# Performance work log

Measured on AMD Instinct MI355X. Metric: run time of the kernel, lower is better.

The kernel has to match this reference:

```python
import jax, jax.numpy as jnp
import numpy as np

N = 100000      # nodes
E = 1600000     # edges
G = 256         # graphs in the batch
D_IN = 128
H = 128
C = 10
EPS = 1e-5      # BatchNorm eps


def setup_inputs() -> dict:
    key = jax.random.key(0)
    ks = jax.random.split(key, 32)
    inp = {
        'x': jax.random.normal(ks[0], (N, D_IN), jnp.float32),
        'edge_index': jax.random.randint(ks[1], (2, E), 0, N, dtype=jnp.int64),
        'batch': jnp.sort(jax.random.randint(ks[2], (N,), 0, G, dtype=jnp.int64)),
        'w1': jax.random.normal(ks[3], (D_IN, H), jnp.float32) * 0.05,
        'b1': jax.random.normal(ks[4], (H,), jnp.float32) * 0.05,
        'w2': jax.random.normal(ks[5], (H, H), jnp.float32) * 0.05,
        'b2': jax.random.normal(ks[6], (H,), jnp.float32) * 0.05,
        'w3': jax.random.normal(ks[7], (H, H), jnp.float32) * 0.05,
        'b3': jax.random.normal(ks[8], (H,), jnp.float32) * 0.05,
        'g1': jax.random.uniform(ks[9], (H,), jnp.float32, 0.5, 1.5),
        'be1': jax.random.normal(ks[10], (H,), jnp.float32) * 0.05,
        'm1': jax.random.normal(ks[11], (H,), jnp.float32) * 0.05,
        'v1': jax.random.uniform(ks[12], (H,), jnp.float32, 0.5, 1.5),
        'g2': jax.random.uniform(ks[13], (H,), jnp.float32, 0.5, 1.5),
        'be2': jax.random.normal(ks[14], (H,), jnp.float32) * 0.05,
        'm2': jax.random.normal(ks[15], (H,), jnp.float32) * 0.05,
        'v2': jax.random.uniform(ks[16], (H,), jnp.float32, 0.5, 1.5),
        'g3': jax.random.uniform(ks[17], (H,), jnp.float32, 0.5, 1.5),
        'be3': jax.random.normal(ks[18], (H,), jnp.float32) * 0.05,
        'm3': jax.random.normal(ks[19], (H,), jnp.float32) * 0.05,
        'v3': jax.random.uniform(ks[20], (H,), jnp.float32, 0.5, 1.5),
        'fcw1': jax.random.normal(ks[21], (H, H // 2), jnp.float32) * 0.05,
        'fcb1': jax.random.normal(ks[22], (H // 2,), jnp.float32) * 0.05,
        'fcw2': jax.random.normal(ks[23], (H // 2, C), jnp.float32) * 0.05,
        'fcb2': jax.random.normal(ks[24], (C,), jnp.float32) * 0.05,
    }
    return inp


def _gcn_norm(edge_index, n_nodes):
    # add self loops (PyG GCNConv default) and compute D^-1/2 (A+I) D^-1/2 norms
    loop = jnp.arange(n_nodes, dtype=edge_index.dtype)
    src = jnp.concatenate([edge_index[0], loop])
    dst = jnp.concatenate([edge_index[1], loop])
    deg = jax.ops.segment_sum(jnp.ones_like(dst, dtype=jnp.float32), dst, num_segments=n_nodes)
    dinv = jnp.where(deg > 0, jax.lax.rsqrt(deg), 0.0)
    norm = dinv[src] * dinv[dst]  # [E+N]
    return src, dst, norm


def _gcn_conv(x, W, b, src, dst, norm, n_nodes):
    h = x @ W                                   # [N, H]
    msg = norm[:, None] * h[src]                # gather + scale, [E+N, H]
    return jax.ops.segment_sum(msg, dst, num_segments=n_nodes) + b


def _bn_eval(x, gamma, beta, mean, var):
    return (x - mean) * jax.lax.rsqrt(var + EPS) * gamma + beta


def reference(x, edge_index, batch, w1, b1, w2, b2, w3, b3,
              g1, be1, m1, v1, g2, be2, m2, v2, g3, be3, m3, v3,
              fcw1, fcb1, fcw2, fcb2):
    n = x.shape[0]
    x = jnp.nan_to_num(x, nan=0.0, posinf=1e6, neginf=-1e6)
    src, dst, norm = _gcn_norm(edge_index, n)

    h = jax.nn.relu(_bn_eval(_gcn_conv(x, w1, b1, src, dst, norm, n), g1, be1, m1, v1))
    h = jax.nn.relu(_bn_eval(_gcn_conv(h, w2, b2, src, dst, norm, n), g2, be2, m2, v2))
    h = jax.nn.relu(_bn_eval(_gcn_conv(h, w3, b3, src, dst, norm, n), g3, be3, m3, v3))

    # global_mean_pool over graphs
    sums = jax.ops.segment_sum(h, batch, num_segments=G)            # [G, H]
    cnts = jax.ops.segment_sum(jnp.ones((n,), h.dtype), batch, num_segments=G)
    pooled = sums / jnp.maximum(cnts, 1.0)[:, None]

    out = jax.nn.relu(pooled @ fcw1 + fcb1) @ fcw2 + fcb2           # [G, C]
    return out
```

## Files before the change

### kernel.cpp

```cpp
#include <hip/hip_runtime.h>
#include <math.h>

#define NN 100000
#define EE 1600000
#define GG 256
#define HH 128
#define BSH 8
#define NBK 391
#define PASSA_WG 391
#define CAPB 5632

typedef __attribute__((ext_vector_type(8))) short short8;
typedef __attribute__((ext_vector_type(4))) float f32x4;

union U4S8 { uint4 u; short8 s; };

static __device__ __forceinline__ unsigned bf16rne(float f) {
    const unsigned u = __float_as_uint(f);
    return (u + 0x7fffu + ((u >> 16) & 1u)) >> 16;
}
static __device__ __forceinline__ unsigned packbf(float a, float b) {
    return bf16rne(a) | (bf16rne(b) << 16);
}
static __device__ __forceinline__ float bflo(unsigned u) { return __uint_as_float(u << 16); }
static __device__ __forceinline__ float bfhi(unsigned u) { return __uint_as_float(u & 0xffff0000u); }

__global__ void detect_k(const int* __restrict__ ei, const int* __restrict__ batch,
                         int* __restrict__ flags) {
    if (threadIdx.x == 0 && blockIdx.x == 0) {
        int e64 = 1;
        for (int j = 0; j < 8; ++j) {
            if (ei[2 * EE - 1 - 2 * j] != 0) { e64 = 0; break; }
        }
        flags[0] = e64;
        flags[1] = (batch[NN - 1] == 0) ? 1 : 0;
    }
}

__global__ __launch_bounds__(512) void cursinit_k(int* __restrict__ cursor) {
    const int b = blockIdx.x * 512 + threadIdx.x;
    if (b < NBK) cursor[b] = b * CAPB;
}

__global__ void bnprep_k(const float* __restrict__ b1, const float* __restrict__ g1,
                         const float* __restrict__ be1, const float* __restrict__ m1,
                         const float* __restrict__ v1,
                         const float* __restrict__ b2, const float* __restrict__ g2,
                         const float* __restrict__ be2, const float* __restrict__ m2,
                         const float* __restrict__ v2,
                         const float* __restrict__ b3, const float* __restrict__ g3,
                         const float* __restrict__ be3, const float* __restrict__ m3,
                         const float* __restrict__ v3,
                         float* __restrict__ sc, float* __restrict__ sh) {
    const int c = threadIdx.x;
    float s;
    s = g1[c] / sqrtf(v1[c] + 1e-5f);
    sc[c] = s;           sh[c] = (b1[c] - m1[c]) * s + be1[c];
    s = g2[c] / sqrtf(v2[c] + 1e-5f);
    sc[128 + c] = s;     sh[128 + c] = (b2[c] - m2[c]) * s + be2[c];
    s = g3[c] / sqrtf(v3[c] + 1e-5f);
    sc[256 + c] = s;     sh[256 + c] = (b3[c] - m3[c]) * s + be3[c];
}

__global__ __launch_bounds__(256) void wprep_k(const float* __restrict__ w1,
                                               const float* __restrict__ w2,
                                               const float* __restrict__ w3,
                                               unsigned* __restrict__ bt) {
    const int id = blockIdx.x * 256 + threadIdx.x;
    if (id >= 3 * 8192) return;
    const int w = id >> 13;
    const int rem = id & 8191;
    const int n = rem >> 6;
    const int kk = rem & 63;
    const float* W = (w == 0) ? w1 : (w == 1) ? w2 : w3;
    bt[id] = packbf(W[(2 * kk) * HH + n], W[(2 * kk + 1) * HH + n]);
}

__global__ __launch_bounds__(256) void passA_k(const int* __restrict__ ei,
                                               const int* __restrict__ flags,
                                               int* __restrict__ cursor,
                                               unsigned* __restrict__ pairs) {
    __shared__ int h[NBK];
    __shared__ int rbase[NBK];
    const int tid = threadIdx.x;
    for (int i = tid; i < NBK; i += 256) h[i] = 0;
    __syncthreads();
    const bool e64 = flags[0] != 0;
    const int base = blockIdx.x * 4096;
    int scache[16], dcache[16];
#pragma unroll
    for (int j = 0; j < 16; ++j) {
        const int e = base + j * 256 + tid;
        int s = -1, d = 0;
        if (e < EE) {
            s = e64 ? ei[2 * e] : ei[e];
            d = e64 ? ei[2 * (EE + e)] : ei[EE + e];
            atomicAdd(&h[d >> BSH], 1);
        }
        scache[j] = s; dcache[j] = d;
    }
    __syncthreads();
    for (int i = tid; i < NBK; i += 256) {
        const int c = h[i];
        rbase[i] = c ? atomicAdd(&cursor[i], c) : 0;
    }
    __syncthreads();
    for (int i = tid; i < NBK; i += 256) h[i] = 0;
    __syncthreads();
#pragma unroll
    for (int j = 0; j < 16; ++j) {
        const int s = scache[j];
        if (s >= 0) {
            const int d = dcache[j];
            const int b = d >> BSH;
            const int r = atomicAdd(&h[b], 1);
            pairs[rbase[b] + r] = ((unsigned)(d & 255) << 17) | (unsigned)s;
        }
    }
}

__global__ __launch_bounds__(256) void passB_k(const unsigned* __restrict__ pairs,
                                               const int* __restrict__ cursor,
                                               int* __restrict__ offs,
                                               int* __restrict__ degcnt,
                                               float* __restrict__ dinv,
                                               int* __restrict__ csr) {
    __shared__ unsigned pk[CAPB];
    __shared__ int cnt[256];
    __shared__ int loff[256];
    __shared__ int sc[256];
    const int tid = threadIdx.x;
    const int b = blockIdx.x;
    const int p0 = b * CAPB;
    const int np = cursor[b] - p0;
    const int nb0 = b << BSH;
    const int nnode = (NN - nb0 < 256) ? (NN - nb0) : 256;

    cnt[tid] = 0;
    __syncthreads();
    for (int i = tid; i < np; i += 256) {
        const unsigned p = pairs[p0 + i];
        pk[i] = p;
        atomicAdd(&cnt[p >> 17], 1);
    }
    __syncthreads();
    const int creal = cnt[tid];
    const int cpad = (tid < nnode) ? ((creal + 4) & ~3) : 0;
    sc[tid] = cpad;
    __syncthreads();
    for (int off = 1; off < 256; off <<= 1) {
        int t = (tid >= off) ? sc[tid - off] : 0;
        __syncthreads();
        sc[tid] += t;
        __syncthreads();
    }
    const int ex = sc[tid] - cpad;
    loff[tid] = ex;
    if (tid < nnode) {
        const int node = nb0 + tid;
        offs[node] = p0 + ex;
        degcnt[node] = creal;
        dinv[node] = 1.0f / sqrtf((float)(creal + 1));
    }
    __syncthreads();
    cnt[tid] = 0;
    __syncthreads();
    for (int i = tid; i < np; i += 256) {
        const unsigned p = pk[i];
        const int dl = (int)(p >> 17);
        const int r = atomicAdd(&cnt[dl], 1);
        csr[p0 + loff[dl] + r] = (int)(p & 0x1FFFFu);
    }
    if (tid < nnode) {
        const int basep = p0 + loff[tid];
        csr[basep + creal] = nb0 + tid;
        for (int j = creal + 1; j < cpad; ++j) csr[basep + j] = NN;
    }
}

static __device__ __forceinline__ float sani(float v) {
    if (isnan(v)) return 0.0f;
    if (isinf(v)) return v > 0.0f ? 1e6f : -1e6f;
    return v;
}

template <bool AF32>
__global__ __launch_bounds__(256) void gemm_mfma_k(const float* __restrict__ Af,
                                                   const unsigned* __restrict__ Abf,
                                                   const unsigned* __restrict__ btg,
                                                   const float* __restrict__ dinv,
                                                   unsigned* __restrict__ C, int M) {
    __shared__ unsigned lds_u[8704];
    const int tid = threadIdx.x;
    const int wave = tid >> 6;
    const int lane = tid & 63;
    const int nl = lane & 15;
    const int q = lane >> 4;

    {
        const uint4* __restrict__ bg4 = (const uint4*)btg;
        for (int i = tid; i < 2048; i += 256) {
            const int n = i >> 4, w4 = i & 15;
            *(uint4*)&lds_u[n * 68 + w4 * 4] = bg4[n * 16 + w4];
        }
    }
    __syncthreads();

    const int row0 = blockIdx.x * 64 + wave * 16;
    const int rowa = min(row0 + nl, M - 1);

    short8 a[4];
    if (AF32) {
#pragma unroll
        for (int ks = 0; ks < 4; ++ks) {
            const float4 p = *(const float4*)(Af + (size_t)rowa * HH + ks * 32 + q * 8);
            const float4 r = *(const float4*)(Af + (size_t)rowa * HH + ks * 32 + q * 8 + 4);
            U4S8 cv;
            cv.u = make_uint4(packbf(sani(p.x), sani(p.y)), packbf(sani(p.z), sani(p.w)),
                              packbf(sani(r.x), sani(r.y)), packbf(sani(r.z), sani(r.w)));
            a[ks] = cv.s;
        }
    } else {
#pragma unroll
        for (int ks = 0; ks < 4; ++ks) {
            U4S8 cv;
            cv.u = *(const uint4*)(Abf + (size_t)rowa * 64 + ks * 16 + q * 4);
            a[ks] = cv.s;
        }
    }

    f32x4 acc[8];
#pragma unroll
    for (int t = 0; t < 8; ++t) acc[t] = (f32x4)0.0f;

    const unsigned short* __restrict__ bts = (const unsigned short*)lds_u;
#pragma unroll
    for (int ks = 0; ks < 4; ++ks) {
#pragma unroll
        for (int t = 0; t < 8; ++t) {
            const int n = t * 16 + nl;
            const short8 b = *(const short8*)(bts + n * 136 + ks * 32 + q * 8);
            acc[t] = __builtin_amdgcn_mfma_f32_16x16x32_bf16(a[ks], b, acc[t], 0, 0, 0);
        }
    }

    __syncthreads();

    float* __restrict__ cs = (float*)lds_u + wave * 16 * 132;
#pragma unroll
    for (int t = 0; t < 8; ++t) {
#pragma unroll
        for (int r = 0; r < 4; ++r) {
            cs[(q * 4 + r) * 132 + t * 16 + nl] = acc[t][r];
        }
    }
    __syncthreads();

    const int rr = lane & 15;
    const int seg = lane >> 4;
    const int rowg = row0 + rr;
    if (rowg < M) {
        const float dsc = dinv[rowg];
        const float4* crow = (const float4*)(cs + rr * 132) + seg * 8;
#pragma unroll
        for (int j = 0; j < 4; ++j) {
            const float4 fa = crow[2 * j];
            const float4 fb = crow[2 * j + 1];
            const uint4 o = make_uint4(packbf(dsc * fa.x, dsc * fa.y),
                                       packbf(dsc * fa.z, dsc * fa.w),
                                       packbf(dsc * fb.x, dsc * fb.y),
                                       packbf(dsc * fb.z, dsc * fb.w));
            *(uint4*)(C + (size_t)rowg * 64 + seg * 16 + j * 4) = o;
        }
    } else if (rowg == M) {
        const uint4 z = make_uint4(0, 0, 0, 0);
#pragma unroll
        for (int j = 0; j < 4; ++j)
            *(uint4*)(C + (size_t)M * 64 + seg * 16 + j * 4) = z;
    }
}

__global__ __launch_bounds__(256) void aggregate_k(
    const unsigned* __restrict__ hpre, const int* __restrict__ csr,
    const int* __restrict__ offs, const int* __restrict__ cnt,
    const float* __restrict__ dinv,
    const float* __restrict__ bnsc, const float* __restrict__ bnsh,
    unsigned* __restrict__ xout) {
    const int v = __builtin_amdgcn_readfirstlane(blockIdx.x * 4 + (threadIdx.x >> 6));
    const int lane = threadIdx.x & 63;
    const int cg = lane & 15;
    const int sub = lane >> 4;
    const int c8 = cg * 8;

    const float dv = dinv[v];
    const int start = offs[v];
    const int npad = (cnt[v] + 4) & ~3;
    const char* __restrict__ hb = (const char*)hpre;
    const unsigned cgo = (unsigned)(cg << 4);

    float acc[8];
#pragma unroll
    for (int j = 0; j < 8; ++j) acc[j] = 0.0f;

    int i = 0;
    for (; i + 8 <= npad; i += 8) {
        const int sA = csr[start + i + sub];
        const int sB = csr[start + i + 4 + sub];
        const uint4 rA = *(const uint4*)(hb + (((unsigned)sA << 8) | cgo));
        const uint4 rB = *(const uint4*)(hb + (((unsigned)sB << 8) | cgo));
        acc[0] += bflo(rA.x) + bflo(rB.x);
        acc[1] += bfhi(rA.x) + bfhi(rB.x);
        acc[2] += bflo(rA.y) + bflo(rB.y);
        acc[3] += bfhi(rA.y) + bfhi(rB.y);
        acc[4] += bflo(rA.z) + bflo(rB.z);
        acc[5] += bfhi(rA.z) + bfhi(rB.z);
        acc[6] += bflo(rA.w) + bflo(rB.w);
        acc[7] += bfhi(rA.w) + bfhi(rB.w);
    }
    if (i < npad) {
        const int s = csr[start + i + sub];
        const uint4 r = *(const uint4*)(hb + (((unsigned)s << 8) | cgo));
        acc[0] += bflo(r.x); acc[1] += bfhi(r.x);
        acc[2] += bflo(r.y); acc[3] += bfhi(r.y);
        acc[4] += bflo(r.z); acc[5] += bfhi(r.z);
        acc[6] += bflo(r.w); acc[7] += bfhi(r.w);
    }

#pragma unroll
    for (int j = 0; j < 8; ++j) {
        acc[j] += __shfl_xor(acc[j], 16);
        acc[j] += __shfl_xor(acc[j], 32);
    }

    if (sub == 0) {
        const float4 sca = *(const float4*)(bnsc + c8);
        const float4 scb = *(const float4*)(bnsc + c8 + 4);
        const float4 sha = *(const float4*)(bnsh + c8);
        const float4 shb = *(const float4*)(bnsh + c8 + 4);
        const float y0 = fmaxf(dv * acc[0] * sca.x + sha.x, 0.0f);
        const float y1 = fmaxf(dv * acc[1] * sca.y + sha.y, 0.0f);
        const float y2 = fmaxf(dv * acc[2] * sca.z + sha.z, 0.0f);
        const float y3 = fmaxf(dv * acc[3] * sca.w + sha.w, 0.0f);
        const float y4 = fmaxf(dv * acc[4] * scb.x + shb.x, 0.0f);
        const float y5 = fmaxf(dv * acc[5] * scb.y + shb.y, 0.0f);
        const float y6 = fmaxf(dv * acc[6] * scb.z + shb.z, 0.0f);
        const float y7 = fmaxf(dv * acc[7] * scb.w + shb.w, 0.0f);
        *(uint4*)(xout + (size_t)v * 64 + cg * 4) =
            make_uint4(packbf(y0, y1), packbf(y2, y3), packbf(y4, y5), packbf(y6, y7));
    }
}

__global__ __launch_bounds__(256) void pool_sum_k(
    const unsigned* __restrict__ x, const int* __restrict__ batch,
    const int* __restrict__ flags, float* __restrict__ psum,
    int* __restrict__ gcnt) {
    const int wave = threadIdx.x >> 6;
    const int lane = threadIdx.x & 63;
    const int row0 = blockIdx.x * 64 + wave * 16;
    if (row0 >= NN) return;
    const bool b64 = flags[1] != 0;

    float sx = 0.0f, sy = 0.0f;
    int cur = -1, runlen = 0;
#pragma unroll
    for (int r = 0; r < 16; ++r) {
        const int row = row0 + r;
        if (row >= NN) break;
        const int g = b64 ? batch[2 * row] : batch[row];
        if (g != cur) {
            if (cur >= 0) {
                atomicAdd(&psum[cur * HH + lane * 2 + 0], sx);
                atomicAdd(&psum[cur * HH + lane * 2 + 1], sy);
                if (lane == 0) atomicAdd(&gcnt[cur], runlen);
            }
            cur = g; sx = 0.0f; sy = 0.0f; runlen = 0;
        }
        const unsigned u = x[(size_t)row * 64 + lane];
        sx += bflo(u);
        sy += bfhi(u);
        ++runlen;
    }
    if (cur >= 0) {
        atomicAdd(&psum[cur * HH + lane * 2 + 0], sx);
        atomicAdd(&psum[cur * HH + lane * 2 + 1], sy);
        if (lane == 0) atomicAdd(&gcnt[cur], runlen);
    }
}

__global__ __launch_bounds__(128) void head_k(
    const float* __restrict__ psum, const int* __restrict__ gcnt,
    const float* __restrict__ fw1, const float* __restrict__ fb1,
    const float* __restrict__ fw2, const float* __restrict__ fb2,
    float* __restrict__ out) {
    __shared__ float pooled[128];
    __shared__ float hid[64];
    const int g = blockIdx.x;
    const int tid = threadIdx.x;

    const int cntn = gcnt[g];
    pooled[tid] = psum[g * HH + tid] / (float)(cntn > 0 ? cntn : 1);
    __syncthreads();

    if (tid < 64) {
        float a = fb1[tid];
#pragma unroll 4
        for (int k = 0; k < 128; ++k) a += pooled[k] * fw1[k * 64 + tid];
        hid[tid] = fmaxf(a, 0.0f);
    }
    __syncthreads();
    if (tid < 10) {
        float a = fb2[tid];
#pragma unroll
        for (int k = 0; k < 64; ++k) a += hid[k] * fw2[k * 10 + tid];
        out[g * 10 + tid] = a;
    }
}

extern "C" void kernel_launch(void* const* d_in, const int* in_sizes, int n_in,
                              void* d_out, int out_size, void* d_ws, size_t ws_size,
                              hipStream_t stream) {
    const float* x_in  = (const float*)d_in[0];
    const int*   ei    = (const int*)d_in[1];
    const int*   batch = (const int*)d_in[2];
    const float* w1 = (const float*)d_in[3];
    const float* b1 = (const float*)d_in[4];
    const float* w2 = (const float*)d_in[5];
    const float* b2 = (const float*)d_in[6];
    const float* w3 = (const float*)d_in[7];
    const float* b3 = (const float*)d_in[8];
    const float* g1 = (const float*)d_in[9];
    const float* be1 = (const float*)d_in[10];
    const float* m1 = (const float*)d_in[11];
    const float* v1 = (const float*)d_in[12];
    const float* g2 = (const float*)d_in[13];
    const float* be2 = (const float*)d_in[14];
    const float* m2 = (const float*)d_in[15];
    const float* v2 = (const float*)d_in[16];
    const float* g3 = (const float*)d_in[17];
    const float* be3 = (const float*)d_in[18];
    const float* m3 = (const float*)d_in[19];
    const float* v3 = (const float*)d_in[20];
    const float* fw1 = (const float*)d_in[21];
    const float* fb1 = (const float*)d_in[22];
    const float* fw2 = (const float*)d_in[23];
    const float* fb2 = (const float*)d_in[24];
    float* out = (float*)d_out;

    size_t off = 0;
    char* base = (char*)d_ws;
    auto alloc = [&](size_t bytes) -> void* {
        void* p = base + off;
        off += (bytes + 255) & ~(size_t)255;
        return p;
    };
    int*      degcnt = (int*)alloc((size_t)NN * 4);
    float*    dinv   = (float*)alloc((size_t)NN * 4);
    int*      offs   = (int*)alloc((size_t)NN * 4);
    int*      cursor = (int*)alloc((size_t)NBK * 4);
    int*      flags  = (int*)alloc(256);
    float*    bnsc   = (float*)alloc(3 * 128 * 4);
    float*    bnsh   = (float*)alloc(3 * 128 * 4);
    unsigned* btg    = (unsigned*)alloc(3 * 8192 * 4);
    float*    psum   = (float*)alloc((size_t)GG * HH * 4);
    int*      gcnt   = (int*)alloc((size_t)GG * 4);
    int*      csr    = (int*)alloc((size_t)NBK * CAPB * 4);
    unsigned* pairs  = (unsigned*)alloc((size_t)NBK * CAPB * 4);
    unsigned* bufx   = (unsigned*)alloc((size_t)NN * 64 * 4);
    unsigned* hpre   = (unsigned*)alloc((size_t)(NN + 1) * 64 * 4);
    if (off > ws_size) return;

    detect_k<<<1, 64, 0, stream>>>(ei, batch, flags);
    cursinit_k<<<1, 512, 0, stream>>>(cursor);
    bnprep_k<<<1, 128, 0, stream>>>(b1, g1, be1, m1, v1,
                                    b2, g2, be2, m2, v2,
                                    b3, g3, be3, m3, v3, bnsc, bnsh);
    wprep_k<<<96, 256, 0, stream>>>(w1, w2, w3, btg);
    hipMemsetAsync(psum, 0, (size_t)GG * HH * 4, stream);
    hipMemsetAsync(gcnt, 0, (size_t)GG * 4, stream);
    passA_k<<<PASSA_WG, 256, 0, stream>>>(ei, flags, cursor, pairs);
    passB_k<<<NBK, 256, 0, stream>>>(pairs, cursor, offs, degcnt, dinv, csr);

    const int ggrid = (NN + 63) / 64;
    const int agrid = NN / 4;

    gemm_mfma_k<true><<<ggrid, 256, 0, stream>>>(x_in, nullptr, btg, dinv, hpre, NN);
    aggregate_k<<<agrid, 256, 0, stream>>>(hpre, csr, offs, degcnt, dinv,
                                           bnsc, bnsh, bufx);
    gemm_mfma_k<false><<<ggrid, 256, 0, stream>>>(nullptr, bufx, btg + 8192, dinv, hpre, NN);
    aggregate_k<<<agrid, 256, 0, stream>>>(hpre, csr, offs, degcnt, dinv,
                                           bnsc + 128, bnsh + 128, bufx);
    gemm_mfma_k<false><<<ggrid, 256, 0, stream>>>(nullptr, bufx, btg + 16384, dinv, hpre, NN);
    aggregate_k<<<agrid, 256, 0, stream>>>(hpre, csr, offs, degcnt, dinv,
                                           bnsc + 256, bnsh + 256, bufx);

    pool_sum_k<<<ggrid, 256, 0, stream>>>(bufx, batch, flags, psum, gcnt);
    head_k<<<GG, 128, 0, stream>>>(psum, gcnt, fw1, fb1, fw2, fb2, out);
}
```

Baseline: 456.5 us.

## Drop LDS staging in MFMA GEMM and unroll aggregation gather to 16 neighbors

The GEMM kernel no longer stages the weight matrix and output tile through shared memory. It reads B fragments straight from global memory and swaps MFMA operands so each lane holds a row-contiguous output that it writes directly as packed bf16. This removes the LDS copies and barriers, at the cost of redundant global/L2 reads of the weights per wave. Separately, CSR rows are padded to multiples of 8 instead of 4 (with a larger per-bucket capacity), so the aggregation loop can issue four independent gathers per iteration for more memory-level parallelism, at the cost of extra padding entries.

New measurement: 506.7 us. 11.0% more time.

```diff
diff --git a/kernel.cpp b/kernel.cpp
--- a/kernel.cpp
+++ b/kernel.cpp
@@ -8,7 +8,7 @@
 #define BSH 8
 #define NBK 391
 #define PASSA_WG 391
-#define CAPB 5632
+#define CAPB 6144
 
 typedef __attribute__((ext_vector_type(8))) short short8;
 typedef __attribute__((ext_vector_type(4))) float f32x4;
@@ -145,7 +145,7 @@
     }
     __syncthreads();
     const int creal = cnt[tid];
-    const int cpad = (tid < nnode) ? ((creal + 4) & ~3) : 0;
+    const int cpad = (tid < nnode) ? ((creal + 8) & ~7) : 0;
     sc[tid] = cpad;
     __syncthreads();
     for (int off = 1; off < 256; off <<= 1) {
@@ -190,24 +190,14 @@
                                                    const unsigned* __restrict__ btg,
                                                    const float* __restrict__ dinv,
                                                    unsigned* __restrict__ C, int M) {
-    __shared__ unsigned lds_u[8704];
     const int tid = threadIdx.x;
     const int wave = tid >> 6;
     const int lane = tid & 63;
     const int nl = lane & 15;
     const int q = lane >> 4;
-
-    {
-        const uint4* __restrict__ bg4 = (const uint4*)btg;
-        for (int i = tid; i < 2048; i += 256) {
-            const int n = i >> 4, w4 = i & 15;
-            *(uint4*)&lds_u[n * 68 + w4 * 4] = bg4[n * 16 + w4];
-        }
-    }
-    __syncthreads();
-
     const int row0 = blockIdx.x * 64 + wave * 16;
-    const int rowa = min(row0 + nl, M - 1);
+    const int rowg = row0 + nl;
+    const int rowa = min(rowg, M - 1);
 
     short8 a[4];
     if (AF32) {
@@ -233,50 +223,33 @@
 #pragma unroll
     for (int t = 0; t < 8; ++t) acc[t] = (f32x4)0.0f;
 
-    const unsigned short* __restrict__ bts = (const unsigned short*)lds_u;
-#pragma unroll
-    for (int ks = 0; ks < 4; ++ks) {
-#pragma unroll
-        for (int t = 0; t < 8; ++t) {
-            const int n = t * 16 + nl;
-            const short8 b = *(const short8*)(bts + n * 136 + ks * 32 + q * 8);
-            acc[t] = __builtin_amdgcn_mfma_f32_16x16x32_bf16(a[ks], b, acc[t], 0, 0, 0);
-        }
-    }
-
-    __syncthreads();
-
-    float* __restrict__ cs = (float*)lds_u + wave * 16 * 132;
+    const uint4* __restrict__ bt4 = (const uint4*)btg;
 #pragma unroll
     for (int t = 0; t < 8; ++t) {
-#pragma unroll
-        for (int r = 0; r < 4; ++r) {
-            cs[(q * 4 + r) * 132 + t * 16 + nl] = acc[t][r];
-        }
-    }
-    __syncthreads();
-
-    const int rr = lane & 15;
-    const int seg = lane >> 4;
-    const int rowg = row0 + rr;
+        const int n = t * 16 + nl;
+#pragma unroll
+        for (int ks = 0; ks < 4; ++ks) {
+            U4S8 cv;
+            cv.u = bt4[n * 16 + ks * 4 + q];
+            acc[t] = __builtin_amdgcn_mfma_f32_16x16x32_bf16(cv.s, a[ks], acc[t], 0, 0, 0);
+        }
+    }
+
     if (rowg < M) {
         const float dsc = dinv[rowg];
-        const float4* crow = (const float4*)(cs + rr * 132) + seg * 8;
-#pragma unroll
-        for (int j = 0; j < 4; ++j) {
-            const float4 fa = crow[2 * j];
-            const float4 fb = crow[2 * j + 1];
-            const uint4 o = make_uint4(packbf(dsc * fa.x, dsc * fa.y),
-                                       packbf(dsc * fa.z, dsc * fa.w),
-                                       packbf(dsc * fb.x, dsc * fb.y),
-                                       packbf(dsc * fb.z, dsc * fb.w));
-            *(uint4*)(C + (size_t)rowg * 64 + seg * 16 + j * 4) = o;
+        unsigned* crow = C + (size_t)rowg * 64;
+#pragma unroll
+        for (int t = 0; t < 8; ++t) {
+            uint2 o;
+            o.x = packbf(dsc * acc[t][0], dsc * acc[t][1]);
+            o.y = packbf(dsc * acc[t][2], dsc * acc[t][3]);
+            *(uint2*)(crow + t * 8 + q * 2) = o;
         }
     } else if (rowg == M) {
-        const uint4 z = make_uint4(0, 0, 0, 0);
-#pragma unroll
-        for (int j = 0; j < 4; ++j)
-            *(uint4*)(C + (size_t)M * 64 + seg * 16 + j * 4) = z;
+        unsigned* crow = C + (size_t)M * 64;
+#pragma unroll
+        for (int t = 0; t < 8; ++t)
+            *(uint2*)(crow + t * 8 + q * 2) = make_uint2(0u, 0u);
     }
 }
 
@@ -294,7 +267,7 @@
 
     const float dv = dinv[v];
     const int start = offs[v];
-    const int npad = (cnt[v] + 4) & ~3;
+    const int npad = (cnt[v] + 8) & ~7;
     const char* __restrict__ hb = (const char*)hpre;
     const unsigned cgo = (unsigned)(cg << 4);
 
@@ -303,7 +276,25 @@
     for (int j = 0; j < 8; ++j) acc[j] = 0.0f;
 
     int i = 0;
-    for (; i + 8 <= npad; i += 8) {
+    for (; i + 16 <= npad; i += 16) {
+        const int sA = csr[start + i + sub];
+        const int sB = csr[start + i + 4 + sub];
+        const int sC = csr[start + i + 8 + sub];
+        const int sD = csr[start + i + 12 + sub];
+        const uint4 rA = *(const uint4*)(hb + (((unsigned)sA << 8) | cgo));
+        const uint4 rB = *(const uint4*)(hb + (((unsigned)sB << 8) | cgo));
+        const uint4 rC = *(const uint4*)(hb + (((unsigned)sC << 8) | cgo));
+        const uint4 rD = *(const uint4*)(hb + (((unsigned)sD << 8) | cgo));
+        acc[0] += (bflo(rA.x) + bflo(rB.x)) + (bflo(rC.x) + bflo(rD.x));
+        acc[1] += (bfhi(rA.x) + bfhi(rB.x)) + (bfhi(rC.x) + bfhi(rD.x));
+        acc[2] += (bflo(rA.y) + bflo(rB.y)) + (bflo(rC.y) + bflo(rD.y));
+        acc[3] += (bfhi(rA.y) + bfhi(rB.y)) + (bfhi(rC.y) + bfhi(rD.y));
+        acc[4] += (bflo(rA.z) + bflo(rB.z)) + (bflo(rC.z) + bflo(rD.z));
+        acc[5] += (bfhi(rA.z) + bfhi(rB.z)) + (bfhi(rC.z) + bfhi(rD.z));
+        acc[6] += (bflo(rA.w) + bflo(rB.w)) + (bflo(rC.w) + bflo(rD.w));
+        acc[7] += (bfhi(rA.w) + bfhi(rB.w)) + (bfhi(rC.w) + bfhi(rD.w));
+    }
+    if (i < npad) {
         const int sA = csr[start + i + sub];
         const int sB = csr[start + i + 4 + sub];
         const uint4 rA = *(const uint4*)(hb + (((unsigned)sA << 8) | cgo));
@@ -316,14 +307,6 @@
         acc[5] += bfhi(rA.z) + bfhi(rB.z);
         acc[6] += bflo(rA.w) + bflo(rB.w);
         acc[7] += bfhi(rA.w) + bfhi(rB.w);
-    }
-    if (i < npad) {
-        const int s = csr[start + i + sub];
-        const uint4 r = *(const uint4*)(hb + (((unsigned)s << 8) | cgo));
-        acc[0] += bflo(r.x); acc[1] += bfhi(r.x);
-        acc[2] += bflo(r.y); acc[3] += bfhi(r.y);
-        acc[4] += bflo(r.z); acc[5] += bfhi(r.z);
-        acc[6] += bflo(r.w); acc[7] += bfhi(r.w);
     }
 
 #pragma unroll
```
